# Performance work log

Measured on AMD Instinct MI355X. Metric: run time of the kernel, lower is better.

## Reference

```python
import jax, jax.numpy as jnp
import numpy as np

N_EMBD = 1184
N_HEAD = 8
D_K = N_EMBD // N_HEAD  # 148
B, T = 4, 2048


def setup_inputs() -> dict:
    key = jax.random.key(0)
    ks = jax.random.split(key, 5)
    scale = 1.0 / np.sqrt(N_EMBD)
    return {
        "x": jax.random.normal(ks[0], (B, T, N_EMBD), dtype=jnp.float32),
        "w_attn": jax.random.normal(ks[1], (3 * N_EMBD, N_EMBD), dtype=jnp.float32) * scale,
        "b_attn": jax.random.normal(ks[2], (3 * N_EMBD,), dtype=jnp.float32) * 0.01,
        "w_proj": jax.random.normal(ks[3], (N_EMBD, N_EMBD), dtype=jnp.float32) * scale,
        "b_proj": jax.random.normal(ks[4], (N_EMBD,), dtype=jnp.float32) * 0.01,
    }


def reference(x, w_attn, b_attn, w_proj, b_proj):
    Bb, Tt, C = x.shape
    # fused qkv projection: [B,T,3C]
    qkv = x @ w_attn.T + b_attn
    q, k, v = jnp.split(qkv, 3, axis=-1)
    # [B, H, T, d_k]
    q = q.reshape(Bb, Tt, N_HEAD, D_K).transpose(0, 2, 1, 3)
    k = k.reshape(Bb, Tt, N_HEAD, D_K).transpose(0, 2, 1, 3)
    v = v.reshape(Bb, Tt, N_HEAD, D_K).transpose(0, 2, 1, 3)
    # scaled scores [B,H,T,T]
    scores = jnp.einsum("bhqd,bhkd->bhqk", q, k) * (1.0 / np.sqrt(D_K))
    causal = jnp.tril(jnp.ones((Tt, Tt), dtype=bool))
    scores = jnp.where(causal, scores, -jnp.inf)
    attn = jax.nn.softmax(scores, axis=-1)
    y = jnp.einsum("bhqk,bhkd->bhqd", attn, v)
    y = y.transpose(0, 2, 1, 3).reshape(Bb, Tt, C)
    return y @ w_proj.T + b_proj
```

## Files before the change

kernel.cpp:

```cpp
#include <hip/hip_runtime.h>
#include <stdint.h>

#define B_ 4
#define H_ 8
#define T_ 2048
#define C_ 1184
#define DK_ 148
#define DP_ 160
#define C3_ 3552

typedef __attribute__((ext_vector_type(8))) short s8v;
typedef __attribute__((ext_vector_type(4))) short s4v;
typedef __attribute__((ext_vector_type(4))) float f4v;
typedef __attribute__((ext_vector_type(16))) float f16v;

#define CSC 0.11858886f

__device__ __forceinline__ unsigned short f2b(float f) {
  union { float f; unsigned u; } v; v.f = f;
  unsigned r = v.u + 0x7FFFu + ((v.u >> 16) & 1u);
  return (unsigned short)(r >> 16);
}

__device__ __forceinline__ void gld16(const void* g, void* l) {
  __builtin_amdgcn_global_load_lds(
      (const __attribute__((address_space(1))) void*)g,
      (__attribute__((address_space(3))) void*)l, 16, 0, 0);
}

__global__ __launch_bounds__(256) void cvt4(const float* __restrict__ src,
                                            short* __restrict__ dst, int n4) {
  int i = blockIdx.x * 256 + threadIdx.x;
  if (i >= n4) return;
  float4 f = ((const float4*)src)[i];
  s4v o = { (short)f2b(f.x), (short)f2b(f.y), (short)f2b(f.z), (short)f2b(f.w) };
  ((s4v*)dst)[i] = o;
}

__global__ __launch_bounds__(256) void zpad(short* __restrict__ Qb,
                                            short* __restrict__ Kb) {
  const int row = blockIdx.x * 256 + threadIdx.x;
  const size_t off = (size_t)row * DP_ + DK_;
  const s4v z = { 0, 0, 0, 0 };
  *(s4v*)(Qb + off) = z; *(s4v*)(Qb + off + 4) = z; *(s4v*)(Qb + off + 8) = z;
  *(s4v*)(Kb + off) = z; *(s4v*)(Kb + off + 4) = z; *(s4v*)(Kb + off + 8) = z;
}

template <int EPI, int NT>
__global__ __launch_bounds__(256, 2) void gemm_bt(
    const short* __restrict__ A, const short* __restrict__ Bm,
    const float* __restrict__ bias,
    short* __restrict__ Qb, short* __restrict__ Kb, short* __restrict__ Vt,
    float* __restrict__ Out) {
  constexpr int K = C_;
  constexpr int NK = K / 32;
  __shared__ short As[2][128 * 32];
  __shared__ short Bs[2][128 * 32];
  const int tid = threadIdx.x;
  const int lane = tid & 63;
  const int wid = tid >> 6;
  const int lo = lane & 15, hi = lane >> 4;
  const int bid = blockIdx.x;
  const int xcd = bid & 7;
  const int kk = bid >> 3;
  const int m0 = (xcd * 8 + kk / NT) * 128;
  const int n0 = (kk % NT) * 128;
  const int wr = wid >> 1, wc = wid & 1;

  const int r0 = tid >> 2;
  const int sg = (tid & 3) * 8;
  const short* pa0 = A + (size_t)(m0 + r0) * K + sg;
  const short* pa1 = A + (size_t)(m0 + r0 + 64) * K + sg;
  const short* pb0 = Bm + (size_t)(n0 + r0) * K + sg;
  const short* pb1 = Bm + (size_t)(n0 + r0 + 64) * K + sg;

  f4v acc[4][4] = {};

#define STAGE(kk_, buf)                               \
  do {                                                \
    const int _o = (kk_) * 32;                        \
    gld16(pa0 + _o, &As[(buf)][tid * 8]);             \
    gld16(pa1 + _o, &As[(buf)][(tid + 256) * 8]);     \
    gld16(pb0 + _o, &Bs[(buf)][tid * 8]);             \
    gld16(pb1 + _o, &Bs[(buf)][(tid + 256) * 8]);     \
  } while (0)

  STAGE(0, 0);
  int cur = 0;
  for (int ks = 0; ks < NK; ++ks) {
    __syncthreads();
    if (ks + 1 < NK) STAGE(ks + 1, cur ^ 1);
    const short* Ab = As[cur];
    const short* Bb = Bs[cur];
    s8v af[4], bf[4];
#pragma unroll
    for (int m = 0; m < 4; ++m)
      af[m] = *(const s8v*)&Ab[(wr * 64 + m * 16 + lo) * 32 + hi * 8];
#pragma unroll
    for (int n = 0; n < 4; ++n)
      bf[n] = *(const s8v*)&Bb[(wc * 64 + n * 16 + lo) * 32 + hi * 8];
#pragma unroll
    for (int m = 0; m < 4; ++m)
#pragma unroll
      for (int n = 0; n < 4; ++n)
        acc[m][n] = __builtin_amdgcn_mfma_f32_16x16x32_bf16(af[m], bf[n], acc[m][n], 0, 0, 0);
    cur ^= 1;
  }
#undef STAGE

#pragma unroll
  for (int n = 0; n < 4; ++n) {
    const int gn = n0 + wc * 64 + n * 16 + lo;
    if (EPI == 0) {
      if (gn < C3_) {
        const float bv = bias[gn];
        const int sel = gn / C_;
        const int r = gn - sel * C_;
        const int h = r / DK_;
        const int d = r - h * DK_;
#pragma unroll
        for (int m = 0; m < 4; ++m) {
          const int t0 = m0 + wr * 64 + m * 16 + hi * 4;
          const int b = t0 >> 11, tt = t0 & 2047;
          const int bh = b * H_ + h;
          if (sel == 2) {
            s4v o = { (short)f2b(acc[m][n][0] + bv), (short)f2b(acc[m][n][1] + bv),
                      (short)f2b(acc[m][n][2] + bv), (short)f2b(acc[m][n][3] + bv) };
            *(s4v*)&Vt[((size_t)bh * DP_ + d) * T_ + tt] = o;
          } else {
#pragma unroll
            for (int j = 0; j < 4; ++j) {
              const short v = (sel == 0) ? (short)f2b((acc[m][n][j] + bv) * CSC)
                                         : (short)f2b(acc[m][n][j] + bv);
              if (sel == 0) Qb[((size_t)bh * T_ + tt + j) * DP_ + d] = v;
              else          Kb[((size_t)bh * T_ + tt + j) * DP_ + d] = v;
            }
          }
        }
      }
    } else {
      if (gn < C_) {
        const float bv = bias[gn];
#pragma unroll
        for (int m = 0; m < 4; ++m)
#pragma unroll
          for (int j = 0; j < 4; ++j) {
            const int gm = m0 + wr * 64 + m * 16 + hi * 4 + j;
            Out[(size_t)gm * C_ + gn] = acc[m][n][j] + bv;
          }
      }
    }
  }
}

__global__ __launch_bounds__(256, 2) void attn(
    const short* __restrict__ Qb, const short* __restrict__ Kb,
    const short* __restrict__ Vt, short* __restrict__ Y) {
  __shared__ short Ks[2][10240];
  __shared__ short Vs[2][10240];
  const int tid = threadIdx.x;
  const int lane = tid & 63;
  const int wid = tid >> 6;
  const int q31 = lane & 31;
  const int h32 = lane >> 5;
  const int s = blockIdx.x;
  const int xcd = s & 7;
  const int k = s >> 3;
  int qb, bsub;
  if (k < 32) { bsub = k >> 4; qb = k & 15; }
  else { bsub = 2 + ((k - 32) >> 4); qb = 15 - (k & 15); }
  const int bh = xcd * 4 + bsub;
  const int q0 = qb * 128 + wid * 32;
  const short* Qh = Qb + (size_t)bh * T_ * DP_;
  const short* Kh = Kb + (size_t)bh * T_ * DP_;
  const short* Vh = Vt + (size_t)bh * DP_ * T_;

  s8v qf[10];
#pragma unroll
  for (int c = 0; c < 10; ++c)
    qf[c] = *(const s8v*)(Qh + (size_t)(q0 + q31) * DP_ + c * 16 + h32 * 8);

  f16v acc[5] = {};
  float mrun = -INFINITY, lrun = 0.f;
  const int nt = 2 * (qb + 1);

#define STAGEKV(kt_, buf_)                                                   \
  do {                                                                       \
    const size_t kvo_ = (size_t)(kt_) * 64;                                  \
    _Pragma("unroll")                                                        \
    for (int i_ = 0; i_ < 5; ++i_) {                                         \
      const int g_ = tid + i_ * 256;                                         \
      const int c_ = g_ >> 8, re_ = g_ & 255, r_ = re_ >> 2, wz_ = re_ & 3;  \
      const int w_ = wz_ ^ ((r_ >> 1) & 3);                                  \
      gld16(Kh + (kvo_ + r_) * DP_ + c_ * 32 + w_ * 8, &Ks[buf_][g_ * 8]);   \
      const int d_ = g_ >> 3, vz_ = g_ & 7;                                  \
      const int v_ = vz_ ^ (d_ & 7);                                         \
      gld16(Vh + (size_t)d_ * T_ + kvo_ + v_ * 8, &Vs[buf_][g_ * 8]);        \
    }                                                                        \
  } while (0)

  STAGEKV(0, 0);
  int cur = 0;
  for (int kt = 0; kt < nt; ++kt) {
    __syncthreads();
    if (kt + 1 < nt) STAGEKV(kt + 1, cur ^ 1);
    const int kv0 = kt * 64;
    if (kv0 <= q0 + 31) {
      const short* Kc = Ks[cur];
      const short* Vc = Vs[cur];
      f16v sc[2] = {};
      __builtin_amdgcn_s_setprio(1);
#pragma unroll
      for (int t2 = 0; t2 < 2; ++t2) {
        const int r_ = t2 * 32 + q31;
#pragma unroll
        for (int c16 = 0; c16 < 10; ++c16) {
          const int u_ = 2 * c16 + h32;
          const int w_ = (u_ & 3) ^ ((r_ >> 1) & 3);
          s8v kf = *(const s8v*)&Kc[((u_ >> 2) * 256 + r_ * 4 + w_) * 8];
          sc[t2] = __builtin_amdgcn_mfma_f32_32x32x16_bf16(kf, qf[c16], sc[t2], 0, 0, 0);
        }
      }
      __builtin_amdgcn_s_setprio(0);
      const int qrow = q0 + q31;
      if (kv0 + 63 > q0) {
#pragma unroll
        for (int t2 = 0; t2 < 2; ++t2)
#pragma unroll
          for (int g = 0; g < 4; ++g)
#pragma unroll
            for (int j = 0; j < 4; ++j)
              if (kv0 + t2 * 32 + 8 * g + 4 * h32 + j > qrow)
                sc[t2][4 * g + j] = -INFINITY;
      }
      float tm = -INFINITY;
#pragma unroll
      for (int t2 = 0; t2 < 2; ++t2)
#pragma unroll
        for (int r = 0; r < 16; ++r) tm = fmaxf(tm, sc[t2][r]);
      tm = fmaxf(tm, __shfl_xor(tm, 32));
      if (!__all(tm <= mrun + 8.f)) {
        const float nm = fmaxf(mrun, tm);
        const float corr = exp2f(mrun - nm);
        mrun = nm;
        lrun *= corr;
#pragma unroll
        for (int dt = 0; dt < 5; ++dt)
#pragma unroll
          for (int r = 0; r < 16; ++r) acc[dt][r] *= corr;
      }
      float ps = 0.f;
#pragma unroll
      for (int t2 = 0; t2 < 2; ++t2)
#pragma unroll
        for (int r = 0; r < 16; ++r) {
          sc[t2][r] = exp2f(sc[t2][r] - mrun);
          ps += sc[t2][r];
        }
      ps += __shfl_xor(ps, 32);
      lrun += ps;
#pragma unroll
      for (int st = 0; st < 4; ++st) {
        const int t2 = st >> 1, g4 = (st & 1) * 8;
        unsigned wA0 = (unsigned)f2b(sc[t2][g4 + 0]) | ((unsigned)f2b(sc[t2][g4 + 1]) << 16);
        unsigned wA1 = (unsigned)f2b(sc[t2][g4 + 2]) | ((unsigned)f2b(sc[t2][g4 + 3]) << 16);
        unsigned wB0 = (unsigned)f2b(sc[t2][g4 + 4]) | ((unsigned)f2b(sc[t2][g4 + 5]) << 16);
        unsigned wB1 = (unsigned)f2b(sc[t2][g4 + 6]) | ((unsigned)f2b(sc[t2][g4 + 7]) << 16);
        const unsigned sxA0 = (unsigned)__shfl_xor((int)wA0, 32);
        const unsigned sxA1 = (unsigned)__shfl_xor((int)wA1, 32);
        const unsigned sxB0 = (unsigned)__shfl_xor((int)wB0, 32);
        const unsigned sxB1 = (unsigned)__shfl_xor((int)wB1, 32);
        union { unsigned w[4]; s8v v; } pf;
        pf.w[0] = h32 ? sxB0 : wA0;
        pf.w[1] = h32 ? sxB1 : wA1;
        pf.w[2] = h32 ? wB0 : sxA0;
        pf.w[3] = h32 ? wB1 : sxA1;
        __builtin_amdgcn_s_setprio(1);
#pragma unroll
        for (int dt = 0; dt < 5; ++dt) {
          const int d_ = dt * 32 + q31;
          const int sl_ = (st * 2 + h32) ^ (d_ & 7);
          s8v vf = *(const s8v*)&Vc[(d_ * 8 + sl_) * 8];
          acc[dt] = __builtin_amdgcn_mfma_f32_32x32x16_bf16(vf, pf.v, acc[dt], 0, 0, 0);
        }
        __builtin_amdgcn_s_setprio(0);
      }
    }
    cur ^= 1;
  }
#undef STAGEKV

  const float inv = 1.0f / lrun;
  const int b = bh >> 3, h = bh & 7;
  const int trow = q0 + q31;
  const size_t ybase = ((size_t)(b * T_ + trow)) * C_ + h * DK_;
#pragma unroll
  for (int dt = 0; dt < 5; ++dt)
#pragma unroll
    for (int g = 0; g < 4; ++g) {
      const int d0 = dt * 32 + 8 * g + 4 * h32;
      if (d0 + 3 < DK_) {
        s4v o = { (short)f2b(acc[dt][4 * g + 0] * inv), (short)f2b(acc[dt][4 * g + 1] * inv),
                  (short)f2b(acc[dt][4 * g + 2] * inv), (short)f2b(acc[dt][4 * g + 3] * inv) };
        *(s4v*)(Y + ybase + d0) = o;
      }
    }
}

extern "C" void kernel_launch(void* const* d_in, const int* in_sizes, int n_in,
                              void* d_out, int out_size, void* d_ws, size_t ws_size,
                              hipStream_t stream) {
  const float* x  = (const float*)d_in[0];
  const float* wA = (const float*)d_in[1];
  const float* bA = (const float*)d_in[2];
  const float* wP = (const float*)d_in[3];
  const float* bP = (const float*)d_in[4];
  float* out = (float*)d_out;

  short* ws  = (short*)d_ws;
  short* xb  = ws;
  short* wab = xb + 9699328;
  short* wpb = wab + 4243456;
  short* Qb  = wpb + 1515520;
  short* Kb  = Qb + 10485760;
  short* Vt  = Kb + 10485760;

  cvt4<<<(9699328 / 4 + 255) / 256, 256, 0, stream>>>(x, xb, 9699328 / 4);
  cvt4<<<(4205568 / 4 + 255) / 256, 256, 0, stream>>>(wA, wab, 4205568 / 4);
  cvt4<<<(1401856 / 4 + 255) / 256, 256, 0, stream>>>(wP, wpb, 1401856 / 4);
  zpad<<<256, 256, 0, stream>>>(Qb, Kb);

  gemm_bt<0, 28><<<1792, 256, 0, stream>>>(xb, wab, bA, Qb, Kb, Vt, nullptr);
  attn<<<512, 256, 0, stream>>>(Qb, Kb, Vt, xb);
  gemm_bt<1, 10><<<640, 256, 0, stream>>>(xb, wpb, bP, nullptr, nullptr, nullptr, out);
}
```

Measured before the change: 250.7 us.

## Add 256x256-tile 8-wave QKV GEMM with triple-buffered swizzled LDS pipeline

Replaces the 128x128 QKV projection GEMM with a new 512-thread kernel that computes 256x256 tiles. It uses a three-stage LDS ring with an XOR swizzle on the shared-memory layout, splits each K step into two MFMA phases interleaved with prefetch, and raises MFMA priority with setprio. Larger tiles raise arithmetic intensity and cut global re-reads, while the swizzle targets LDS bank conflicts. In exchange it needs more LDS (about 96KB) and more registers, and launches only 448 blocks, which may lower occupancy and give poor wave balance across CUs.

```diff
diff --git a/kernel.cpp b/kernel.cpp
--- a/kernel.cpp
+++ b/kernel.cpp
@@ -46,12 +46,140 @@
   *(s4v*)(Kb + off) = z; *(s4v*)(Kb + off + 4) = z; *(s4v*)(Kb + off + 8) = z;
 }
 
-template <int EPI, int NT>
+#define SWZ(r) ((((r) & 3) ^ (((r) >> 2) & 3)))
+template <int NT>
+__global__ __launch_bounds__(512, 2) void gemm_qkv8(
+    const short* __restrict__ A, const short* __restrict__ Bm,
+    const float* __restrict__ bias,
+    short* __restrict__ Qb, short* __restrict__ Kb, short* __restrict__ Vt) {
+  constexpr int NKT = C_ / 32;
+  __shared__ short As[3][256 * 32];
+  __shared__ short Bs[3][256 * 32];
+  const int tid = threadIdx.x;
+  const int lane = tid & 63;
+  const int wid = tid >> 6;
+  const int lo = lane & 15, hi = lane >> 4;
+  const int wr = wid >> 2, wc = wid & 3;
+  const int bid = blockIdx.x;
+  const int xcd = bid & 7, kk = bid >> 3;
+  const int m0 = (xcd * 4 + kk / NT) * 256;
+  const int n0 = (kk % NT) * 256;
+
+  const int rS = tid >> 2, uS = tid & 3;
+  const int seg = (uS ^ SWZ(rS)) * 8;
+  const short* paw0 = A + (size_t)(m0 + rS) * C_ + seg;
+  const short* paw1 = A + (size_t)(m0 + rS + 128) * C_ + seg;
+  const short* pbw0 = Bm + (size_t)(n0 + rS) * C_ + seg;
+  const short* pbw1 = Bm + (size_t)(n0 + rS + 128) * C_ + seg;
+
+#define STGA(kk_, buf_)                                   \
+  do {                                                    \
+    gld16(paw0 + (kk_) * 32, &As[buf_][tid * 8]);         \
+    gld16(paw1 + (kk_) * 32, &As[buf_][(tid + 512) * 8]); \
+  } while (0)
+#define STGB(kk_, buf_)                                   \
+  do {                                                    \
+    gld16(pbw0 + (kk_) * 32, &Bs[buf_][tid * 8]);         \
+    gld16(pbw1 + (kk_) * 32, &Bs[buf_][(tid + 512) * 8]); \
+  } while (0)
+
+  f4v acc[8][4] = {};
+  const int swzl = SWZ(lo);
+
+  STGA(0, 0); STGB(0, 0);
+  STGA(1, 1); STGB(1, 1);
+  asm volatile("s_waitcnt vmcnt(4)" ::: "memory");
+  __builtin_amdgcn_s_barrier();
+
+  int cur = 0;
+  for (int t = 0; t < NKT; ++t) {
+    const short* Ab = As[cur];
+    const short* Bb = Bs[cur];
+    int nxt = cur + 2; if (nxt >= 3) nxt -= 3;
+    const bool pf = (t + 2 < NKT);
+
+    s8v af[4], bf[4];
+#pragma unroll
+    for (int m = 0; m < 4; ++m) {
+      const int r = wr * 128 + m * 16 + lo;
+      af[m] = *(const s8v*)&Ab[(r * 4 + (hi ^ swzl)) * 8];
+    }
+#pragma unroll
+    for (int n = 0; n < 4; ++n) {
+      const int r = wc * 64 + n * 16 + lo;
+      bf[n] = *(const s8v*)&Bb[(r * 4 + (hi ^ swzl)) * 8];
+    }
+    if (pf) STGA(t + 2, nxt);
+    __builtin_amdgcn_s_barrier();
+    __builtin_amdgcn_s_setprio(1);
+#pragma unroll
+    for (int m = 0; m < 4; ++m)
+#pragma unroll
+      for (int n = 0; n < 4; ++n)
+        acc[m][n] = __builtin_amdgcn_mfma_f32_16x16x32_bf16(af[m], bf[n], acc[m][n], 0, 0, 0);
+    __builtin_amdgcn_s_setprio(0);
+    __builtin_amdgcn_s_barrier();
+
+    s8v ag[4];
+#pragma unroll
+    for (int m = 0; m < 4; ++m) {
+      const int r = wr * 128 + 64 + m * 16 + lo;
+      ag[m] = *(const s8v*)&Ab[(r * 4 + (hi ^ swzl)) * 8];
+    }
+    if (pf) STGB(t + 2, nxt);
+    __builtin_amdgcn_s_barrier();
+    __builtin_amdgcn_s_setprio(1);
+#pragma unroll
+    for (int m = 0; m < 4; ++m)
+#pragma unroll
+      for (int n = 0; n < 4; ++n)
+        acc[m + 4][n] = __builtin_amdgcn_mfma_f32_16x16x32_bf16(ag[m], bf[n], acc[m + 4][n], 0, 0, 0);
+    __builtin_amdgcn_s_setprio(0);
+    if (pf) asm volatile("s_waitcnt vmcnt(4)" ::: "memory");
+    else    asm volatile("s_waitcnt vmcnt(0)" ::: "memory");
+    __builtin_amdgcn_s_barrier();
+    cur = (cur + 1 == 3) ? 0 : cur + 1;
+  }
+#undef STGA
+#undef STGB
+
+#pragma unroll
+  for (int n = 0; n < 4; ++n) {
+    const int gn = n0 + wc * 64 + n * 16 + lo;
+    if (gn < C3_) {
+      const float bv = bias[gn];
+      const int sel = gn / C_;
+      const int r = gn - sel * C_;
+      const int h = r / DK_;
+      const int d = r - h * DK_;
+#pragma unroll
+      for (int m = 0; m < 8; ++m) {
+        const int t0 = m0 + wr * 128 + ((m & 3) * 16) + ((m >> 2) * 64) + hi * 4;
+        const int b = t0 >> 11, tt = t0 & 2047;
+        const int bh = b * H_ + h;
+        const int mi = (m < 4) ? m : m;
+        if (sel == 2) {
+          s4v o = { (short)f2b(acc[mi][n][0] + bv), (short)f2b(acc[mi][n][1] + bv),
+                    (short)f2b(acc[mi][n][2] + bv), (short)f2b(acc[mi][n][3] + bv) };
+          *(s4v*)&Vt[((size_t)bh * DP_ + d) * T_ + tt] = o;
+        } else {
+#pragma unroll
+          for (int j = 0; j < 4; ++j) {
+            const short v = (sel == 0) ? (short)f2b((acc[mi][n][j] + bv) * CSC)
+                                       : (short)f2b(acc[mi][n][j] + bv);
+            if (sel == 0) Qb[((size_t)bh * T_ + tt + j) * DP_ + d] = v;
+            else          Kb[((size_t)bh * T_ + tt + j) * DP_ + d] = v;
+          }
+        }
+      }
+    }
+  }
+}
+
+template <int NT>
 __global__ __launch_bounds__(256, 2) void gemm_bt(
     const short* __restrict__ A, const short* __restrict__ Bm,
-    const float* __restrict__ bias,
-    short* __restrict__ Qb, short* __restrict__ Kb, short* __restrict__ Vt,
-    float* __restrict__ Out) {
+    const float* __restrict__ bias, float* __restrict__ Out) {
   constexpr int K = C_;
   constexpr int NK = K / 32;
   __shared__ short As[2][128 * 32];
@@ -111,44 +239,15 @@
 #pragma unroll
   for (int n = 0; n < 4; ++n) {
     const int gn = n0 + wc * 64 + n * 16 + lo;
-    if (EPI == 0) {
-      if (gn < C3_) {
-        const float bv = bias[gn];
-        const int sel = gn / C_;
-        const int r = gn - sel * C_;
-        const int h = r / DK_;
-        const int d = r - h * DK_;
-#pragma unroll
-        for (int m = 0; m < 4; ++m) {
-          const int t0 = m0 + wr * 64 + m * 16 + hi * 4;
-          const int b = t0 >> 11, tt = t0 & 2047;
-          const int bh = b * H_ + h;
-          if (sel == 2) {
-            s4v o = { (short)f2b(acc[m][n][0] + bv), (short)f2b(acc[m][n][1] + bv),
-                      (short)f2b(acc[m][n][2] + bv), (short)f2b(acc[m][n][3] + bv) };
-            *(s4v*)&Vt[((size_t)bh * DP_ + d) * T_ + tt] = o;
-          } else {
-#pragma unroll
-            for (int j = 0; j < 4; ++j) {
-              const short v = (sel == 0) ? (short)f2b((acc[m][n][j] + bv) * CSC)
-                                         : (short)f2b(acc[m][n][j] + bv);
-              if (sel == 0) Qb[((size_t)bh * T_ + tt + j) * DP_ + d] = v;
-              else          Kb[((size_t)bh * T_ + tt + j) * DP_ + d] = v;
-            }
-          }
+    if (gn < C_) {
+      const float bv = bias[gn];
+#pragma unroll
+      for (int m = 0; m < 4; ++m)
+#pragma unroll
+        for (int j = 0; j < 4; ++j) {
+          const int gm = m0 + wr * 64 + m * 16 + hi * 4 + j;
+          Out[(size_t)gm * C_ + gn] = acc[m][n][j] + bv;
         }
-      }
-    } else {
-      if (gn < C_) {
-        const float bv = bias[gn];
-#pragma unroll
-        for (int m = 0; m < 4; ++m)
-#pragma unroll
-          for (int j = 0; j < 4; ++j) {
-            const int gm = m0 + wr * 64 + m * 16 + hi * 4 + j;
-            Out[(size_t)gm * C_ + gn] = acc[m][n][j] + bv;
-          }
-      }
     }
   }
 }
@@ -330,7 +429,7 @@
   cvt4<<<(1401856 / 4 + 255) / 256, 256, 0, stream>>>(wP, wpb, 1401856 / 4);
   zpad<<<256, 256, 0, stream>>>(Qb, Kb);
 
-  gemm_bt<0, 28><<<1792, 256, 0, stream>>>(xb, wab, bA, Qb, Kb, Vt, nullptr);
+  gemm_qkv8<14><<<448, 512, 0, stream>>>(xb, wab, bA, Qb, Kb, Vt);
   attn<<<512, 256, 0, stream>>>(Qb, Kb, Vt, xb);
-  gemm_bt<1, 10><<<640, 256, 0, stream>>>(xb, wpb, bP, nullptr, nullptr, nullptr, out);
-}
+  gemm_bt<10><<<640, 256, 0, stream>>>(xb, wpb, bP, out);
+}
```

After: 247.6 us. About the same (-1.3%).

## Add 256x256-tile 8-wave QKV GEMM with 4-stage swizzled LDS pipeline

Applied to the files above, without the earlier changes.

Replaces the 128x128 QKV projection GEMM with a dedicated kernel using 256x256 output tiles, 512 threads, and a four-slot LDS ring. Global-to-LDS loads are interleaved with MFMA phases, and explicit barriers and waitcnts are added around them. An XOR swizzle on the LDS layout is meant to avoid bank conflicts, and wave priority is raised during the MFMA bursts. The aim is more operand reuse per loaded byte and better overlap of loads with math. In exchange it uses 128KB of LDS, which allows only one block per CU, and puts more accumulator pressure on registers. The output projection GEMM keeps its old path, with the epilogue template parameter removed.

```diff
diff --git a/kernel.cpp b/kernel.cpp
--- a/kernel.cpp
+++ b/kernel.cpp
@@ -28,6 +28,13 @@
       (__attribute__((address_space(3))) void*)l, 16, 0, 0);
 }
 
+#define SBAR() asm volatile("s_barrier" ::: "memory")
+#define LGKM0()                                            \
+  do {                                                     \
+    asm volatile("s_waitcnt lgkmcnt(0)" ::: "memory");     \
+    __builtin_amdgcn_sched_barrier(0);                     \
+  } while (0)
+
 __global__ __launch_bounds__(256) void cvt4(const float* __restrict__ src,
                                             short* __restrict__ dst, int n4) {
   int i = blockIdx.x * 256 + threadIdx.x;
@@ -46,12 +53,166 @@
   *(s4v*)(Kb + off) = z; *(s4v*)(Kb + off + 4) = z; *(s4v*)(Kb + off + 8) = z;
 }
 
-template <int EPI, int NT>
+template <int NT>
+__global__ __launch_bounds__(512, 2) void gemm_qkv8(
+    const short* __restrict__ A, const short* __restrict__ Bm,
+    const float* __restrict__ bias,
+    short* __restrict__ Qb, short* __restrict__ Kb, short* __restrict__ Vt) {
+  __shared__ short As[4][8192];
+  __shared__ short Bs[4][8192];
+  const int tid = threadIdx.x;
+  const int lane = tid & 63;
+  const int wid = tid >> 6;
+  const int lo = lane & 15, hi = lane >> 4;
+  const int wr = wid >> 2, wc = wid & 3;
+  const int bid = blockIdx.x;
+  const int xcd = bid & 7, kk = bid >> 3;
+  const int m0 = (xcd * 4 + kk / NT) * 256;
+  const int n0 = (kk % NT) * 256;
+
+  const int rS = tid >> 2;
+  const int gS = (tid & 3) ^ ((rS ^ (rS >> 2)) & 3);
+  const short* pA0 = A + (size_t)(m0 + rS) * C_ + gS * 8;
+  const short* pA1 = A + (size_t)(m0 + rS + 128) * C_ + gS * 8;
+  const short* pB0 = Bm + (size_t)(n0 + rS) * C_ + gS * 8;
+  const short* pB1 = Bm + (size_t)(n0 + rS + 128) * C_ + gS * 8;
+
+#define STG_A(tt, khs, sl)                                      \
+  do {                                                          \
+    const int _o = (tt) * 64 + (khs) * 32;                      \
+    gld16(pA0 + _o, &As[sl][tid * 8]);                          \
+    gld16(pA1 + _o, &As[sl][(tid + 512) * 8]);                  \
+  } while (0)
+#define STG_B(tt, khs, sl)                                      \
+  do {                                                          \
+    const int _o = (tt) * 64 + (khs) * 32;                      \
+    gld16(pB0 + _o, &Bs[sl][tid * 8]);                          \
+    gld16(pB1 + _o, &Bs[sl][(tid + 512) * 8]);                  \
+  } while (0)
+
+  f4v acc[8][4] = {};
+  const int gr = (hi ^ ((lo ^ (lo >> 2)) & 3)) * 8;
+  const int rAb = wr * 128 + lo;
+  const int rBb = wc * 64 + lo;
+
+  STG_A(0, 0, 0); STG_B(0, 0, 0);
+  STG_A(0, 1, 1); STG_B(0, 1, 1);
+  STG_A(1, 0, 2); STG_B(1, 0, 2);
+  asm volatile("s_waitcnt vmcnt(4)" ::: "memory");
+  SBAR();
+
+#define MFMA16(base, bfr)                                                     \
+  do {                                                                        \
+    __builtin_amdgcn_s_setprio(1);                                            \
+    _Pragma("unroll") for (int m = 0; m < 4; ++m)                             \
+      _Pragma("unroll") for (int n = 0; n < 4; ++n)                           \
+        acc[(base) + m][n] = __builtin_amdgcn_mfma_f32_16x16x32_bf16(         \
+            af[m], bfr[n], acc[(base) + m][n], 0, 0, 0);                      \
+    __builtin_amdgcn_s_setprio(0);                                            \
+  } while (0)
+
+  for (int t = 0; t < 18; ++t) {
+    const int s0 = (2 * t) & 3;
+    const int s1 = s0 + 1;
+    const int sN = (s0 + 3) & 3;
+    const bool pf = (t < 17);
+    s8v af[4], bf0[4], bf1[4];
+
+#pragma unroll
+    for (int n = 0; n < 4; ++n)
+      bf0[n] = *(const s8v*)&Bs[s0][(rBb + n * 16) * 32 + gr];
+#pragma unroll
+    for (int m = 0; m < 4; ++m)
+      af[m] = *(const s8v*)&As[s0][(rAb + m * 16) * 32 + gr];
+    if (pf) STG_A(t + 1, 1, sN);
+    SBAR(); LGKM0();
+    MFMA16(0, bf0);
+    SBAR();
+
+#pragma unroll
+    for (int m = 0; m < 4; ++m)
+      af[m] = *(const s8v*)&As[s0][(rAb + 64 + m * 16) * 32 + gr];
+    if (pf) STG_B(t + 1, 1, sN);
+    SBAR(); LGKM0();
+    MFMA16(4, bf0);
+    SBAR();
+
+#pragma unroll
+    for (int n = 0; n < 4; ++n)
+      bf1[n] = *(const s8v*)&Bs[s1][(rBb + n * 16) * 32 + gr];
+#pragma unroll
+    for (int m = 0; m < 4; ++m)
+      af[m] = *(const s8v*)&As[s1][(rAb + m * 16) * 32 + gr];
+    if (pf) STG_A(t + 2, 0, s0);
+    SBAR(); LGKM0();
+    MFMA16(0, bf1);
+    SBAR();
+
+#pragma unroll
+    for (int m = 0; m < 4; ++m)
+      af[m] = *(const s8v*)&As[s1][(rAb + 64 + m * 16) * 32 + gr];
+    if (pf) STG_B(t + 2, 0, s0);
+    SBAR(); LGKM0();
+    MFMA16(4, bf1);
+    if (t < 17) asm volatile("s_waitcnt vmcnt(4)" ::: "memory");
+    else        asm volatile("s_waitcnt vmcnt(0)" ::: "memory");
+    SBAR();
+  }
+
+  {
+    s8v af[4], bfT[4];
+#pragma unroll
+    for (int n = 0; n < 4; ++n)
+      bfT[n] = *(const s8v*)&Bs[0][(rBb + n * 16) * 32 + gr];
+#pragma unroll
+    for (int m = 0; m < 4; ++m)
+      af[m] = *(const s8v*)&As[0][(rAb + m * 16) * 32 + gr];
+    MFMA16(0, bfT);
+#pragma unroll
+    for (int m = 0; m < 4; ++m)
+      af[m] = *(const s8v*)&As[0][(rAb + 64 + m * 16) * 32 + gr];
+    MFMA16(4, bfT);
+  }
+#undef MFMA16
+#undef STG_A
+#undef STG_B
+
+#pragma unroll
+  for (int n = 0; n < 4; ++n) {
+    const int gn = n0 + wc * 64 + n * 16 + lo;
+    if (gn < C3_) {
+      const float bv = bias[gn];
+      const int sel = gn / C_;
+      const int r = gn - sel * C_;
+      const int h = r / DK_;
+      const int d = r - h * DK_;
+#pragma unroll
+      for (int m = 0; m < 8; ++m) {
+        const int t0 = m0 + wr * 128 + (m >> 2) * 64 + (m & 3) * 16 + hi * 4;
+        const int b = t0 >> 11, tt = t0 & 2047;
+        const int bh = b * H_ + h;
+        if (sel == 2) {
+          s4v o = { (short)f2b(acc[m][n][0] + bv), (short)f2b(acc[m][n][1] + bv),
+                    (short)f2b(acc[m][n][2] + bv), (short)f2b(acc[m][n][3] + bv) };
+          *(s4v*)&Vt[((size_t)bh * DP_ + d) * T_ + tt] = o;
+        } else {
+#pragma unroll
+          for (int j = 0; j < 4; ++j) {
+            const short v = (sel == 0) ? (short)f2b((acc[m][n][j] + bv) * CSC)
+                                       : (short)f2b(acc[m][n][j] + bv);
+            if (sel == 0) Qb[((size_t)bh * T_ + tt + j) * DP_ + d] = v;
+            else          Kb[((size_t)bh * T_ + tt + j) * DP_ + d] = v;
+          }
+        }
+      }
+    }
+  }
+}
+
+template <int NT>
 __global__ __launch_bounds__(256, 2) void gemm_bt(
     const short* __restrict__ A, const short* __restrict__ Bm,
-    const float* __restrict__ bias,
-    short* __restrict__ Qb, short* __restrict__ Kb, short* __restrict__ Vt,
-    float* __restrict__ Out) {
+    const float* __restrict__ bias, float* __restrict__ Out) {
   constexpr int K = C_;
   constexpr int NK = K / 32;
   __shared__ short As[2][128 * 32];
@@ -111,44 +272,15 @@
 #pragma unroll
   for (int n = 0; n < 4; ++n) {
     const int gn = n0 + wc * 64 + n * 16 + lo;
-    if (EPI == 0) {
-      if (gn < C3_) {
-        const float bv = bias[gn];
-        const int sel = gn / C_;
-        const int r = gn - sel * C_;
-        const int h = r / DK_;
-        const int d = r - h * DK_;
-#pragma unroll
-        for (int m = 0; m < 4; ++m) {
-          const int t0 = m0 + wr * 64 + m * 16 + hi * 4;
-          const int b = t0 >> 11, tt = t0 & 2047;
-          const int bh = b * H_ + h;
-          if (sel == 2) {
-            s4v o = { (short)f2b(acc[m][n][0] + bv), (short)f2b(acc[m][n][1] + bv),
-                      (short)f2b(acc[m][n][2] + bv), (short)f2b(acc[m][n][3] + bv) };
-            *(s4v*)&Vt[((size_t)bh * DP_ + d) * T_ + tt] = o;
-          } else {
-#pragma unroll
-            for (int j = 0; j < 4; ++j) {
-              const short v = (sel == 0) ? (short)f2b((acc[m][n][j] + bv) * CSC)
-                                         : (short)f2b(acc[m][n][j] + bv);
-              if (sel == 0) Qb[((size_t)bh * T_ + tt + j) * DP_ + d] = v;
-              else          Kb[((size_t)bh * T_ + tt + j) * DP_ + d] = v;
-            }
-          }
+    if (gn < C_) {
+      const float bv = bias[gn];
+#pragma unroll
+      for (int m = 0; m < 4; ++m)
+#pragma unroll
+        for (int j = 0; j < 4; ++j) {
+          const int gm = m0 + wr * 64 + m * 16 + hi * 4 + j;
+          Out[(size_t)gm * C_ + gn] = acc[m][n][j] + bv;
         }
-      }
-    } else {
-      if (gn < C_) {
-        const float bv = bias[gn];
-#pragma unroll
-        for (int m = 0; m < 4; ++m)
-#pragma unroll
-          for (int j = 0; j < 4; ++j) {
-            const int gm = m0 + wr * 64 + m * 16 + hi * 4 + j;
-            Out[(size_t)gm * C_ + gn] = acc[m][n][j] + bv;
-          }
-      }
     }
   }
 }
@@ -330,7 +462,7 @@
   cvt4<<<(1401856 / 4 + 255) / 256, 256, 0, stream>>>(wP, wpb, 1401856 / 4);
   zpad<<<256, 256, 0, stream>>>(Qb, Kb);
 
-  gemm_bt<0, 28><<<1792, 256, 0, stream>>>(xb, wab, bA, Qb, Kb, Vt, nullptr);
+  gemm_qkv8<14><<<448, 512, 0, stream>>>(xb, wab, bA, Qb, Kb, Vt);
   attn<<<512, 256, 0, stream>>>(Qb, Kb, Vt, xb);
-  gemm_bt<1, 10><<<640, 256, 0, stream>>>(xb, wpb, bP, nullptr, nullptr, nullptr, out);
-}
+  gemm_bt<10><<<640, 256, 0, stream>>>(xb, wpb, bP, out);
+}
```

New measurement: 255.3 us. About the same (+1.8%).
